# Optimization experiments

Measured on AMD Instinct MI355X. Metric: run time of the kernel, lower is better.

## Reference

```python
import jax, jax.numpy as jnp
import numpy as np

N, E, C_IN, W = 7936, 63488, 5, 64
K, H1, H2 = 8, 64, 16  # kernel size, tgc hidden, gcn out

def _conv1d(x, w, b):
    # x: [N, Cin, L], w: [Cout, Cin, K] -> [N, Cout, L-K+1]
    y = jax.lax.conv_general_dilated(x, w, (1,), 'VALID',
                                     dimension_numbers=('NCH', 'OIH', 'NCH'))
    return y + b[None, :, None]

def _gated_conv(x, w, b, out_ch):
    # Conv1d to 2*out_ch channels, then GLU: P * sigmoid(Q)
    y = _conv1d(x, w, b)
    return y[:, :out_ch] * jax.nn.sigmoid(y[:, out_ch:])

def _gcn(x, edge_index, edge_weight, Wg, bg, num_nodes):
    # x: [T, N, F] (node_dim=-2), GCNConv with self-loops and symmetric norm
    row, col = edge_index[0], edge_index[1]
    loop = jnp.arange(num_nodes, dtype=edge_index.dtype)
    row = jnp.concatenate([row, loop])
    col = jnp.concatenate([col, loop])
    ew = jnp.concatenate([edge_weight, jnp.ones((num_nodes,), x.dtype)])
    deg = jax.ops.segment_sum(ew, col, num_segments=num_nodes)
    dinv = jnp.where(deg > 0, jax.lax.rsqrt(deg), 0.0)
    norm = dinv[row] * ew * dinv[col]              # [E+N]
    xt = jnp.einsum('tnf,fo->tno', x, Wg)          # transform first (F->O)
    msgs = jnp.take(xt, row, axis=1) * norm[None, :, None]  # [T, E+N, O]
    T = x.shape[0]
    out = jnp.zeros((T, num_nodes, Wg.shape[1]), x.dtype).at[:, col, :].add(msgs)
    return out + bg

def setup_inputs() -> dict:
    key = jax.random.key(0)
    ks = jax.random.split(key, 10)
    x = jax.random.normal(ks[0], (N, C_IN, W), jnp.float32)
    edge_index = jax.random.randint(ks[1], (2, E), 0, N, jnp.int64)
    edge_attr = jax.random.uniform(ks[2], (E,), jnp.float32)
    batch = jax.random.randint(ks[3], (N,), 0, 128, jnp.int64)
    s1 = 1.0 / np.sqrt(C_IN * K)
    Wc1 = jax.random.uniform(ks[4], (2 * H1, C_IN, K), jnp.float32, -s1, s1)
    b1 = jax.random.uniform(ks[5], (2 * H1,), jnp.float32, -s1, s1)
    sg = 1.0 / np.sqrt(H1)
    Wg = jax.random.uniform(ks[6], (H1, H2), jnp.float32, -sg, sg)
    bg = jnp.zeros((H2,), jnp.float32)
    s2 = 1.0 / np.sqrt(H2 * K)
    Wc2 = jax.random.uniform(ks[7], (2 * H1, H2, K), jnp.float32, -s2, s2)
    b2 = jax.random.uniform(ks[8], (2 * H1,), jnp.float32, -s2, s2)
    return {'x': x, 'edge_index': edge_index, 'edge_attr': edge_attr,
            'batch': batch, 'Wc1': Wc1, 'b1': b1, 'Wg': Wg, 'bg': bg,
            'Wc2': Wc2, 'b2': b2}

def reference(x, edge_index, edge_attr, batch, Wc1, b1, Wg, bg, Wc2, b2):
    h = _gated_conv(x, Wc1, b1, H1)                # [N, 64, T1]
    h = jnp.transpose(h, (2, 0, 1))                # 'ec cs wc -> wc ec cs'
    h = jax.nn.relu(_gcn(h, edge_index, edge_attr, Wg, bg, x.shape[0]))
    h = jnp.transpose(h, (1, 2, 0))                # 'wc ec cs -> ec cs wc'
    return _gated_conv(h, Wc2, b2, H1)             # [N, 64, T2]
```

## Files before the change

### kernel.cpp

```cpp
#include <hip/hip_runtime.h>
#include <hip/hip_bf16.h>

#define NN 7936
#define EE 63488
#define CIN 5
#define WW 64
#define KK 8
#define H1C 64
#define H2C 16
#define T1 57
#define T2 50
#define FT (T1*H2C)
#define CAP 64
#define GSTR 24

typedef _Float16 half8 __attribute__((ext_vector_type(8)));
typedef _Float16 half4v __attribute__((ext_vector_type(4)));
typedef float f32x4 __attribute__((ext_vector_type(4)));

__device__ __forceinline__ int block_flag(const int* __restrict__ ei,
                                          int* sflag) {
    if (threadIdx.x < 64) {
        int bad = (threadIdx.x < 32) ? (ei[2 * threadIdx.x + 1] != 0) : 0;
        unsigned long long b = __ballot(bad);
        if (threadIdx.x == 0) *sflag = (b == 0ULL) ? 1 : 0;
    }
    __syncthreads();
    return *sflag;
}

__device__ __forceinline__ int load_row(const int* ei, int f, int e) {
    return f ? ei[2 * e] : ei[e];
}
__device__ __forceinline__ int load_col(const int* ei, int f, int e) {
    return f ? ei[2 * (EE + e)] : ei[EE + e];
}

__global__ void k_init(float* __restrict__ deg,
                       const float* __restrict__ Wc2, _Float16* __restrict__ w2p,
                       const float* __restrict__ Wc1, _Float16* __restrict__ w1p,
                       const float* __restrict__ Wg, _Float16* __restrict__ wgp) {
    int b = blockIdx.x;
    if (b < 62) {
        ((int*)deg)[b * 256 + threadIdx.x] = 0;
        return;
    }
    int i = (b - 62) * 256 + threadIdx.x;
    if (i < 16384) {
        int e = i & 7;
        int slot = i >> 3;
        int c  = slot & 15;
        int nt = (slot >> 4) & 7;
        int g  = (slot >> 7) & 3;
        int s  = (slot >> 9) & 3;
        int ci = g * 4 + (e & 3);
        w2p[i] = (_Float16)Wc2[(nt * 16 + c) * 128 + ci * 8 + 2 * s + (e >> 2)];
    } else if (i < 16384 + 8192) {
        int j = i - 16384;
        int e = j & 7;
        int m = (j >> 3) & 127;
        int slg = j >> 10;
        int ci = (slg >> 2) * 4 + (slg & 3);
        int hi = m >> 6;
        int mb = m & 63;
        int mt = mb >> 4, r = mb & 15;
        int sig = hi * 64 + 32 * (mt >> 1) + 8 * (r >> 2) + 4 * (mt & 1) + (r & 3);
        w1p[j] = (ci < CIN) ? (_Float16)Wc1[sig * (CIN * KK) + ci * KK + e]
                            : (_Float16)0.0f;
    } else if (i < 16384 + 8192 + 1024) {
        int j = i - 16384 - 8192;
        int e = j & 7;
        int f = (j >> 3) & 15;
        int slg = j >> 7;
        int c = (slg >> 2) * 32 + (slg & 3) * 8 + e;
        wgp[j] = (_Float16)Wg[c * H2C + f];
    }
}

__global__ void k_deg(const int* __restrict__ ei, const float* __restrict__ ew,
                      float* __restrict__ deg) {
    __shared__ int sflag;
    int f = block_flag(ei, &sflag);
    int e = blockIdx.x * 256 + threadIdx.x;
    int c = load_col(ei, f, e);
    atomicAdd(&deg[c], ew[e]);
}

__global__ __launch_bounds__(256, 3) void k_conv1_fill(
        const float* __restrict__ x, const _Float16* __restrict__ w1p,
        const float* __restrict__ b1, const _Float16* __restrict__ wgp,
        _Float16* __restrict__ xt,
        const int* __restrict__ ei,
        const float* __restrict__ ew, const float* __restrict__ deg,
        int* __restrict__ cnt, int2* __restrict__ em) {
    if (blockIdx.x >= NN / 4) {
        __shared__ int sflag;
        int f = block_flag(ei, &sflag);
        int e = (blockIdx.x - NN / 4) * 256 + threadIdx.x;
        if (e < EE) {
            int c = load_col(ei, f, e);
            int r = load_row(ei, f, e);
            int pos = atomicAdd(&cnt[c], 1);
            if (pos < CAP)
                em[(c << 6) + pos] =
                    make_int2(r, __float_as_int(rsqrtf(deg[r] + 1.0f) * ew[e]));
        }
        return;
    }
    int tid = threadIdx.x;
    int w = tid >> 6, lane = tid & 63;
    int lc = lane & 15, lg = lane >> 4;
    int n = blockIdx.x * 4 + w;
    const float* xg = x + (size_t)n * (CIN * WW);

    const half8* w1v = (const half8*)w1p;
    const half8* wgv = (const half8*)wgp;

    half8 av[2][8];
#pragma unroll
    for (int s = 0; s < 2; ++s)
#pragma unroll
        for (int mt = 0; mt < 8; ++mt)
            av[s][mt] = w1v[(s * 4 + lg) * 128 + mt * 16 + lc];
    half8 bw[2];
#pragma unroll
    for (int s2 = 0; s2 < 2; ++s2) bw[s2] = wgv[(s2 * 4 + lg) * 16 + lc];

    const float* xr0 = xg + (size_t)lg * WW;
    const float* xr1 = xg + (size_t)(4 + lg) * WW;
    bool cok1 = (4 + lg) < CIN;

    f32x4 acc2[4];
#pragma unroll
    for (int mt2 = 0; mt2 < 4; ++mt2) acc2[mt2] = (f32x4)0.0f;

#pragma unroll
    for (int nt = 0; nt < 4; ++nt) {
        int t = nt * 16 + lc;
        half8 bf0, bf1;
#pragma unroll
        for (int e = 0; e < 8; ++e) {
            int tp = t + e;
            bf0[e] = (_Float16)((tp < WW) ? xr0[tp] : 0.0f);
            bf1[e] = (_Float16)((cok1 && tp < WW) ? xr1[tp] : 0.0f);
        }
        f32x4 acc[8];
#pragma unroll
        for (int mt = 0; mt < 8; ++mt) acc[mt] = (f32x4)0.0f;
#pragma unroll
        for (int mt = 0; mt < 8; ++mt)
            acc[mt] = __builtin_amdgcn_mfma_f32_16x16x32_f16(av[0][mt], bf0,
                                                             acc[mt], 0, 0, 0);
#pragma unroll
        for (int mt = 0; mt < 8; ++mt)
            acc[mt] = __builtin_amdgcn_mfma_f32_16x16x32_f16(av[1][mt], bf1,
                                                             acc[mt], 0, 0, 0);
        half4v h4[4];
#pragma unroll
        for (int mtp = 0; mtp < 4; ++mtp) {
            int cb = 32 * (mtp >> 1) + 8 * lg + 4 * (mtp & 1);
            float4 bP = *(const float4*)(b1 + cb);
            float4 bQ = *(const float4*)(b1 + 64 + cb);
            f32x4 P = acc[mtp];
            f32x4 Q = acc[mtp + 4];
            half4v hh;
            hh[0] = (_Float16)((P[0] + bP.x) * (1.0f / (1.0f + __expf(-(Q[0] + bQ.x)))));
            hh[1] = (_Float16)((P[1] + bP.y) * (1.0f / (1.0f + __expf(-(Q[1] + bQ.y)))));
            hh[2] = (_Float16)((P[2] + bP.z) * (1.0f / (1.0f + __expf(-(Q[2] + bQ.z)))));
            hh[3] = (_Float16)((P[3] + bP.w) * (1.0f / (1.0f + __expf(-(Q[3] + bQ.w)))));
            h4[mtp] = hh;
        }
#pragma unroll
        for (int s2 = 0; s2 < 2; ++s2) {
            half8 af = __builtin_shufflevector(h4[2 * s2], h4[2 * s2 + 1],
                                               0, 1, 2, 3, 4, 5, 6, 7);
            acc2[nt] = __builtin_amdgcn_mfma_f32_16x16x32_f16(af, bw[s2],
                                                              acc2[nt], 0, 0, 0);
        }
    }

    _Float16* xtn = xt + (size_t)n * FT;
#pragma unroll
    for (int mt2 = 0; mt2 < 4; ++mt2) {
#pragma unroll
        for (int j = 0; j < 4; ++j) {
            int t = mt2 * 16 + 4 * lg + j;
            if (t < T1) xtn[t * 16 + lc] = (_Float16)acc2[mt2][j];
        }
    }
}

__global__ __launch_bounds__(256, 4) void k_gc2(
        const _Float16* __restrict__ xt, const float* __restrict__ deg,
        const int* __restrict__ cnt, const int2* __restrict__ em,
        const float* __restrict__ bg, const _Float16* __restrict__ w2p,
        const float* __restrict__ b2, float* __restrict__ out) {
    __shared__ __align__(16) _Float16 gs2[4][58 * GSTR];
    __shared__ __align__(16) float gout[4][16 * T2];
    int tid = threadIdx.x;
    int w = tid >> 6, lane = tid & 63;
    int lc = lane & 15, lg = lane >> 4;
    int n = blockIdx.x * 4 + w;
    bool hi = lane < 50;

    float dc = rsqrtf(deg[n] + 1.0f);
    float a0[8], a1[8];
    {
        const half8* xs = (const half8*)(xt + (size_t)n * FT);
        half8 u0 = xs[lane];
        half8 u1 = (half8)(_Float16)0.0f;
        if (hi) u1 = xs[64 + lane];
        float sw = dc * dc;
#pragma unroll
        for (int j = 0; j < 8; ++j) {
            a0[j] = (float)u0[j] * sw;
            a1[j] = (float)u1[j] * sw;
        }
    }
    int beg = n << 6;
    int m = min(cnt[n], CAP);
    int2 rw0 = make_int2(0, 0), rw1 = make_int2(0, 0);
    half8 c0 = (half8)(_Float16)0.0f, c1 = (half8)(_Float16)0.0f;
    if (m > 0) {
        rw0 = em[beg];
        const half8* xr = (const half8*)(xt + (size_t)rw0.x * FT);
        c0 = xr[lane];
        if (hi) c1 = xr[64 + lane];
    }
    if (m > 1) rw1 = em[beg + 1];
    for (int i = 0; i < m; ++i) {
        float wv = __int_as_float(rw0.y) * dc;
        half8 d0 = c0, d1 = c1;
        int2 rwn = (i + 2 < m) ? em[beg + i + 2] : rw1;
        if (i + 1 < m) {
            const half8* xr = (const half8*)(xt + (size_t)rw1.x * FT);
            c0 = xr[lane];
            c1 = (half8)(_Float16)0.0f;
            if (hi) c1 = xr[64 + lane];
        }
        rw0 = rw1; rw1 = rwn;
#pragma unroll
        for (int j = 0; j < 8; ++j) {
            a0[j] += (float)d0[j] * wv;
            a1[j] += (float)d1[j] * wv;
        }
    }

    {
        _Float16* g = gs2[w];
        int f0 = (lane & 1) * 8;
        int t0 = lane >> 1;
        float4 bgA = *(const float4*)(bg + f0);
        float4 bgB = *(const float4*)(bg + f0 + 4);
        float bv[8] = {bgA.x, bgA.y, bgA.z, bgA.w, bgB.x, bgB.y, bgB.z, bgB.w};
        half8 h0, h1;
#pragma unroll
        for (int j = 0; j < 8; ++j) {
            h0[j] = (_Float16)fmaxf(a0[j] + bv[j], 0.0f);
            h1[j] = (_Float16)fmaxf(a1[j] + bv[j], 0.0f);
        }
        *(half8*)(g + t0 * GSTR + f0) = h0;
        if (hi) *(half8*)(g + (32 + t0) * GSTR + f0) = h1;
    }

    const _Float16* g = gs2[w];
    half8 af[4][4];
#pragma unroll
    for (int s = 0; s < 4; ++s)
#pragma unroll
        for (int mt = 0; mt < 4; ++mt) {
            int tb = mt * 16 + lc + 2 * s;
            half4v lo = *(const half4v*)(g + tb * GSTR + lg * 4);
            half4v hh = *(const half4v*)(g + (tb + 1) * GSTR + lg * 4);
            af[s][mt] = __builtin_shufflevector(lo, hh, 0, 1, 2, 3, 4, 5, 6, 7);
        }

    const half8* wsv = (const half8*)w2p;
    float* outn = out + (size_t)n * (H1C * T2);
    float* go = gout[w];
#pragma unroll
    for (int ntp = 0; ntp < 4; ++ntp) {
        f32x4 aP[4], aQ[4];
#pragma unroll
        for (int mt = 0; mt < 4; ++mt) { aP[mt] = (f32x4)0.0f; aQ[mt] = (f32x4)0.0f; }
#pragma unroll
        for (int s = 0; s < 4; ++s) {
            half8 bP = wsv[(s * 4 + lg) * 128 + ntp * 16 + lc];
            half8 bQ = wsv[(s * 4 + lg) * 128 + (ntp + 4) * 16 + lc];
#pragma unroll
            for (int mt = 0; mt < 4; ++mt) {
                aP[mt] = __builtin_amdgcn_mfma_f32_16x16x32_f16(af[s][mt], bP,
                                                                aP[mt], 0, 0, 0);
                aQ[mt] = __builtin_amdgcn_mfma_f32_16x16x32_f16(af[s][mt], bQ,
                                                                aQ[mt], 0, 0, 0);
            }
        }
        int c = ntp * 16 + lc;
        float bp = b2[c], bq = b2[64 + c];
#pragma unroll
        for (int mt = 0; mt < 4; ++mt) {
#pragma unroll
            for (int e2 = 0; e2 < 4; ++e2) {
                int t = mt * 16 + lg * 4 + e2;
                if (t < T2) {
                    float vv = (aP[mt][e2] + bp) *
                               (1.0f / (1.0f + __expf(-(aQ[mt][e2] + bq))));
                    go[lc * T2 + t] = vv;
                }
            }
        }
        float* dst = outn + ntp * (16 * T2);
#pragma unroll
        for (int i = 0; i < 3; ++i) {
            f32x4 v = *(const f32x4*)(go + i * 256 + lane * 4);
            __builtin_nontemporal_store(v, (f32x4*)(dst + i * 256 + lane * 4));
        }
        if (lane < 8) {
            f32x4 v = *(const f32x4*)(go + 768 + lane * 4);
            __builtin_nontemporal_store(v, (f32x4*)(dst + 768 + lane * 4));
        }
    }
}

extern "C" void kernel_launch(void* const* d_in, const int* in_sizes, int n_in,
                              void* d_out, int out_size, void* d_ws, size_t ws_size,
                              hipStream_t stream) {
    const float* x   = (const float*)d_in[0];
    const int*   ei  = (const int*)d_in[1];
    const float* ea  = (const float*)d_in[2];
    const float* Wc1 = (const float*)d_in[4];
    const float* b1  = (const float*)d_in[5];
    const float* Wg  = (const float*)d_in[6];
    const float* bg  = (const float*)d_in[7];
    const float* Wc2 = (const float*)d_in[8];
    const float* b2  = (const float*)d_in[9];
    float* out = (float*)d_out;

    char* ws = (char*)d_ws;
    size_t off = 0;
    auto alloc = [&](size_t bytes) -> void* {
        void* p = ws + off;
        off += (bytes + 255) & ~(size_t)255;
        return p;
    };
    float*    deg = (float*)alloc((size_t)NN * 4);
    int*      cnt = (int*)alloc((size_t)NN * 4);
    int2*     em  = (int2*)alloc((size_t)NN * CAP * 8);
    _Float16* xt  = (_Float16*)alloc((size_t)NN * FT * 2);
    _Float16* w2p = (_Float16*)alloc((size_t)16384 * 2);
    _Float16* w1p = (_Float16*)alloc((size_t)8192 * 2);
    _Float16* wgp = (_Float16*)alloc((size_t)1024 * 2);
    (void)ws_size; (void)in_sizes; (void)n_in; (void)out_size;

    k_init<<<162, 256, 0, stream>>>(deg, Wc2, w2p, Wc1, w1p, Wg, wgp);
    k_deg<<<EE / 256, 256, 0, stream>>>(ei, ea, deg);
    k_conv1_fill<<<NN / 4 + EE / 256, 256, 0, stream>>>(x, w1p, b1, wgp, xt,
                                                        ei, ea, deg, cnt, em);
    k_gc2<<<NN / 4, 256, 0, stream>>>(xt, deg, cnt, em, bg, w2p, b2, out);
}
```

Before: 103.8 us.

## Split each node's gather and conv2 across two waves in k_gc2

k_gc2 now uses two waves per node instead of one. Each wave gathers half of the node's 114 half8 feature chunks from its neighbors, and the two halves are joined in shared memory with a block barrier. Each wave then computes half of the output channel tiles of the second gated conv. This doubles the grid and halves per-wave registers and serial work. The costs are a __syncthreads, duplicated edge-list and index loads per wave, and idle lanes (14 of 64) in the second wave during the gather.

```diff
diff --git a/kernel.cpp b/kernel.cpp
--- a/kernel.cpp
+++ b/kernel.cpp
@@ -195,75 +195,66 @@
         const int* __restrict__ cnt, const int2* __restrict__ em,
         const float* __restrict__ bg, const _Float16* __restrict__ w2p,
         const float* __restrict__ b2, float* __restrict__ out) {
-    __shared__ __align__(16) _Float16 gs2[4][58 * GSTR];
+    __shared__ __align__(16) _Float16 gs2[2][58 * GSTR];
     __shared__ __align__(16) float gout[4][16 * T2];
     int tid = threadIdx.x;
     int w = tid >> 6, lane = tid & 63;
     int lc = lane & 15, lg = lane >> 4;
-    int n = blockIdx.x * 4 + w;
-    bool hi = lane < 50;
+    int nb = w >> 1, h = w & 1;
+    int n = blockIdx.x * 2 + nb;
+    bool act = (h == 0) || (lane < 50);
+    int idx = (h << 6) + lane;
 
     float dc = rsqrtf(deg[n] + 1.0f);
-    float a0[8], a1[8];
+    float a[8];
     {
         const half8* xs = (const half8*)(xt + (size_t)n * FT);
-        half8 u0 = xs[lane];
-        half8 u1 = (half8)(_Float16)0.0f;
-        if (hi) u1 = xs[64 + lane];
+        half8 u = (half8)(_Float16)0.0f;
+        if (act) u = xs[idx];
         float sw = dc * dc;
 #pragma unroll
-        for (int j = 0; j < 8; ++j) {
-            a0[j] = (float)u0[j] * sw;
-            a1[j] = (float)u1[j] * sw;
-        }
+        for (int j = 0; j < 8; ++j) a[j] = (float)u[j] * sw;
     }
     int beg = n << 6;
     int m = min(cnt[n], CAP);
     int2 rw0 = make_int2(0, 0), rw1 = make_int2(0, 0);
-    half8 c0 = (half8)(_Float16)0.0f, c1 = (half8)(_Float16)0.0f;
+    half8 c0 = (half8)(_Float16)0.0f;
     if (m > 0) {
         rw0 = em[beg];
         const half8* xr = (const half8*)(xt + (size_t)rw0.x * FT);
-        c0 = xr[lane];
-        if (hi) c1 = xr[64 + lane];
+        if (act) c0 = xr[idx];
     }
     if (m > 1) rw1 = em[beg + 1];
     for (int i = 0; i < m; ++i) {
         float wv = __int_as_float(rw0.y) * dc;
-        half8 d0 = c0, d1 = c1;
+        half8 d0 = c0;
         int2 rwn = (i + 2 < m) ? em[beg + i + 2] : rw1;
         if (i + 1 < m) {
             const half8* xr = (const half8*)(xt + (size_t)rw1.x * FT);
-            c0 = xr[lane];
-            c1 = (half8)(_Float16)0.0f;
-            if (hi) c1 = xr[64 + lane];
+            c0 = (half8)(_Float16)0.0f;
+            if (act) c0 = xr[idx];
         }
         rw0 = rw1; rw1 = rwn;
 #pragma unroll
-        for (int j = 0; j < 8; ++j) {
-            a0[j] += (float)d0[j] * wv;
-            a1[j] += (float)d1[j] * wv;
-        }
+        for (int j = 0; j < 8; ++j) a[j] += (float)d0[j] * wv;
     }
 
     {
-        _Float16* g = gs2[w];
+        _Float16* g = gs2[nb];
         int f0 = (lane & 1) * 8;
-        int t0 = lane >> 1;
+        int t0 = idx >> 1;
         float4 bgA = *(const float4*)(bg + f0);
         float4 bgB = *(const float4*)(bg + f0 + 4);
         float bv[8] = {bgA.x, bgA.y, bgA.z, bgA.w, bgB.x, bgB.y, bgB.z, bgB.w};
-        half8 h0, h1;
-#pragma unroll
-        for (int j = 0; j < 8; ++j) {
-            h0[j] = (_Float16)fmaxf(a0[j] + bv[j], 0.0f);
-            h1[j] = (_Float16)fmaxf(a1[j] + bv[j], 0.0f);
-        }
-        *(half8*)(g + t0 * GSTR + f0) = h0;
-        if (hi) *(half8*)(g + (32 + t0) * GSTR + f0) = h1;
-    }
-
-    const _Float16* g = gs2[w];
+        half8 h0;
+#pragma unroll
+        for (int j = 0; j < 8; ++j)
+            h0[j] = (_Float16)fmaxf(a[j] + bv[j], 0.0f);
+        if (act) *(half8*)(g + t0 * GSTR + f0) = h0;
+    }
+    __syncthreads();
+
+    const _Float16* g = gs2[nb];
     half8 af[4][4];
 #pragma unroll
     for (int s = 0; s < 4; ++s)
@@ -279,7 +270,8 @@
     float* outn = out + (size_t)n * (H1C * T2);
     float* go = gout[w];
 #pragma unroll
-    for (int ntp = 0; ntp < 4; ++ntp) {
+    for (int np2 = 0; np2 < 2; ++np2) {
+        int ntp = (h << 1) + np2;
         f32x4 aP[4], aQ[4];
 #pragma unroll
         for (int mt = 0; mt < 4; ++mt) { aP[mt] = (f32x4)0.0f; aQ[mt] = (f32x4)0.0f; }
@@ -356,5 +348,5 @@
     k_deg<<<EE / 256, 256, 0, stream>>>(ei, ea, deg);
     k_conv1_fill<<<NN / 4 + EE / 256, 256, 0, stream>>>(x, w1p, b1, wgp, xt,
                                                         ei, ea, deg, cnt, em);
-    k_gc2<<<NN / 4, 256, 0, stream>>>(xt, deg, cnt, em, bg, w2p, b2, out);
-}
+    k_gc2<<<NN / 2, 256, 0, stream>>>(xt, deg, cnt, em, bg, w2p, b2, out);
+}
```

Result: slower. 108.3 us (+4.3%).
